# Kernel optimization log

Measured on AMD Instinct MI355X. Metric: run time of the kernel, lower is better.

## Reference

```python
import jax, jax.numpy as jnp
import numpy as np

N = 100000      # nodes
E = 3200000     # edges (avg degree 32)
DU = 256        # unary_channels
DP = 256        # pairwise_channels (== out_channels, required by fusion cat)
H = 64          # hidden_channels = out_channels // 4
DO = 256        # out_channels
STEPS = 1
EPS = 1e-5      # BatchNorm eps (torch default)


def _bn(h, gamma, beta):
    # BatchNorm1d, training-mode batch stats (biased variance, as torch normalizes)
    mu = jnp.mean(h, axis=0)
    var = jnp.var(h, axis=0)
    return gamma * (h - mu) * jax.lax.rsqrt(var + EPS) + beta


def setup_inputs() -> dict:
    key = jax.random.key(0)
    ks = jax.random.split(key, 12)
    edge_index = jax.random.randint(ks[0], (2, E), 0, N, dtype=jnp.int64)
    return {
        "x": jax.random.normal(ks[1], (N, DU), dtype=jnp.float32),
        "y": jax.random.normal(ks[2], (N, DP), dtype=jnp.float32),
        "pos": jax.random.normal(ks[3], (N, 3), dtype=jnp.float32),
        "edge_index": edge_index,
        "Wu": jax.random.normal(ks[4], (DU, H), dtype=jnp.float32) / np.sqrt(DU),
        "gu": jnp.ones((H,), jnp.float32), "bu": jnp.zeros((H,), jnp.float32),
        "Wp": jax.random.normal(ks[5], (DP, H), dtype=jnp.float32) / np.sqrt(DP),
        "gp": jnp.ones((H,), jnp.float32), "bp": jnp.zeros((H,), jnp.float32),
        "c": jnp.eye(H, dtype=jnp.float32) + 0.1 * jax.random.normal(ks[6], (H, H), dtype=jnp.float32),
        "Wm": jax.random.normal(ks[7], (H, DO), dtype=jnp.float32) / np.sqrt(H),
        "gm": jnp.ones((DO,), jnp.float32), "bm": jnp.zeros((DO,), jnp.float32),
        "Wf": jax.random.normal(ks[8], (2 * DO, DO), dtype=jnp.float32) / np.sqrt(2 * DO),
        "gf": jnp.ones((DO,), jnp.float32), "bf": jnp.zeros((DO,), jnp.float32),
    }


def reference(x, y, pos, edge_index, Wu, gu, bu, Wp, gp, bp, c, Wm, gm, bm, Wf, gf, bf):
    i, j = edge_index[0], edge_index[1]
    # unary / pairwise embeddings (Linear no-bias + BN)
    xu = _bn(x @ Wu, gu, bu)                      # [N, H]
    su = _bn(y @ Wp, gp, bp)                      # [N, H]
    # edge logits: -||s_i - s_j||^2, softmax grouped by destination i
    d = su[i] - su[j]                             # [E, H]
    logit = -jnp.sum(d * d, axis=1, keepdims=True)  # [E, 1]
    m = jax.ops.segment_max(logit, i, num_segments=N)
    ex = jnp.exp(logit - m[i])
    denom = jax.ops.segment_sum(ex, i, num_segments=N)
    s = ex / (denom[i] + 1e-16)                   # [E, 1] edge softmax weights
    # CRF mean-field iterations with linear solve
    z = xu
    C = c.T @ c                                   # [H, H]
    Minv = jnp.linalg.inv(jnp.eye(H, dtype=x.dtype) + C)
    h = xu
    for _ in range(STEPS):
        agg = jax.ops.segment_sum(s * h[j], i, num_segments=N)  # gather-scale-scatter
        h = (z + agg @ C) @ Minv
    # output heads
    h = jax.nn.leaky_relu(_bn(h @ Wm, gm, bm))
    out = jax.nn.leaky_relu(_bn(jnp.concatenate([h, y], axis=-1) @ Wf, gf, bf))
    return out
```

## Files before the change

### kernel.cpp

```cpp
#include <hip/hip_runtime.h>
#include <hip/hip_fp16.h>
#include <math.h>

typedef unsigned short u16;
typedef short s16x8 __attribute__((ext_vector_type(8)));
typedef unsigned short u16x8 __attribute__((ext_vector_type(8)));
typedef float f32x4 __attribute__((ext_vector_type(4)));

__device__ __forceinline__ float bf2f(u16 u) {
  unsigned x = ((unsigned)u) << 16;
  return __uint_as_float(x);
}
__device__ __forceinline__ u16 f2bf(float f) {
  unsigned x = __float_as_uint(f);
  unsigned r = x + 0x7FFFu + ((x >> 16) & 1u);
  return (u16)(r >> 16);
}

static const size_t OFF_MINV   = 0;
static const size_t OFF_AU     = 32ull * 1024;
static const size_t OFF_BUE    = 32ull * 1024 + 256;
static const size_t OFF_AP     = 32ull * 1024 + 512;
static const size_t OFF_APBE   = 32ull * 1024 + 768;
static const size_t OFF_AM     = 36ull * 1024;
static const size_t OFF_BM     = 37ull * 1024;
static const size_t OFF_AF     = 38ull * 1024;
static const size_t OFF_BF     = 39ull * 1024;
static const size_t OFF_BTOT   = 40ull * 1024;
static const size_t OFF_BOFF   = 44ull * 1024;
static const size_t OFF_WUT    = 64ull * 1024;
static const size_t OFF_WMT    = 128ull * 1024;
static const size_t OFF_WFT    = 192ull * 1024;
static const size_t OFF_WPH    = 512ull * 1024;
static const size_t OFF_WPL    = 576ull * 1024;
static const size_t OFF_PART1  = 1ull  * 1024 * 1024;
static const size_t OFF_PART2  = 2ull  * 1024 * 1024;
static const size_t OFF_ROWPTR = 3ull  * 1024 * 1024;
static const size_t OFF_BLKCNT = 5ull  * 1024 * 1024;
static const size_t OFF_SRCJ   = 18ull * 1024 * 1024;
static const size_t OFF_U      = 44ull * 1024 * 1024;
static const size_t OFF_P      = 70ull * 1024 * 1024;
static const size_t OFF_PS     = 109ull * 1024 * 1024;
static const size_t OFF_H2     = 122ull * 1024 * 1024;

#define NBLK_BIN 1024

__global__ __launch_bounds__(256) void k_prep(const float* __restrict__ c,
                                              float* __restrict__ minv_out) {
  __shared__ float CC[4096];
  __shared__ float aug[64 * 129];
  __shared__ float fs[64];
  float* cl = aug;
  int t = threadIdx.x;
  for (int idx = t; idx < 4096; idx += 256) cl[idx] = c[idx];
  __syncthreads();
  for (int idx = t; idx < 4096; idx += 256) {
    int a = idx >> 6, b = idx & 63;
    float s = (a == b) ? 1.f : 0.f;
    for (int k = 0; k < 64; ++k) s += cl[k * 64 + a] * cl[k * 64 + b];
    CC[idx] = s;
  }
  __syncthreads();
  for (int idx = t; idx < 8192; idx += 256) {
    int r = idx >> 7, cc = idx & 127;
    aug[r * 129 + cc] = (cc < 64) ? CC[r * 64 + cc] : (((cc - 64) == r) ? 1.f : 0.f);
  }
  __syncthreads();
  int cloc = t & 127;
  int rbase = t >> 7;
  for (int p = 0; p < 64; ++p) {
    float inv = 1.0f / aug[p * 129 + p];
    if (t < 64) fs[t] = (t == p) ? 0.f : aug[t * 129 + p];
    __syncthreads();
    if (t < 128) aug[p * 129 + t] *= inv;
    __syncthreads();
    float pc = aug[p * 129 + cloc];
#pragma unroll
    for (int rr = 0; rr < 64; rr += 2) {
      int r = rr + rbase;
      aug[r * 129 + cloc] -= fs[r] * pc;
    }
    __syncthreads();
  }
  for (int idx = t; idx < 4096; idx += 256) {
    int r = idx >> 6, cc = idx & 63;
    minv_out[idx] = aug[r * 129 + 64 + cc];
  }
}

__global__ __launch_bounds__(256) void k_tcvt_all(const float* __restrict__ Wu, const float* __restrict__ Wm,
                                                  const float* __restrict__ Wf, const float* __restrict__ Wp,
                                                  u16* __restrict__ WUT, u16* __restrict__ WMT,
                                                  u16* __restrict__ WFT, u16* __restrict__ WPH,
                                                  u16* __restrict__ WPL) {
  int b = blockIdx.x, t = threadIdx.x;
  if (b < 64) {
    int i = b * 256 + t;
    int k = i >> 6, n = i & 63;
    WUT[(size_t)n * 256 + k] = f2bf(Wu[i]);
  } else if (b < 128) {
    int i = (b - 64) * 256 + t;
    int k = i >> 8, n = i & 255;
    WMT[(size_t)n * 64 + k] = f2bf(Wm[i]);
  } else if (b < 640) {
    int i = (b - 128) * 256 + t;
    int k = i >> 8, n = i & 255;
    WFT[(size_t)n * 512 + k] = f2bf(Wf[i]);
  } else {
    int i = (b - 640) * 256 + t;
    int k = i >> 6, n = i & 63;
    float v = Wp[i];
    u16 h = f2bf(v);
    WPH[(size_t)n * 256 + k] = h;
    WPL[(size_t)n * 256 + k] = f2bf(v - bf2f(h));
  }
}

__global__ __launch_bounds__(256) void kA1(const int* __restrict__ ei, int E, int chunk,
                                           int* __restrict__ blockCnt, int nbk) {
  __shared__ int c[512];
  int t = threadIdx.x, bid = blockIdx.x;
  c[t] = 0; c[t + 256] = 0;
  __syncthreads();
  int e0 = bid * chunk, e1 = min(E, e0 + chunk);
  for (int e = e0 + t; e < e1; e += 256) atomicAdd(&c[ei[e] >> 8], 1);
  __syncthreads();
  for (int b = t; b < nbk; b += 256) blockCnt[(size_t)bid * nbk + b] = c[b];
}

__global__ __launch_bounds__(256) void kA2(int* __restrict__ blockCnt, int nbk,
                                           int* __restrict__ bucketTot) {
  int b = blockIdx.x, t = threadIdx.x;
  int base = t * 4;
  int v0 = blockCnt[(size_t)(base + 0) * nbk + b];
  int v1 = blockCnt[(size_t)(base + 1) * nbk + b];
  int v2 = blockCnt[(size_t)(base + 2) * nbk + b];
  int v3 = blockCnt[(size_t)(base + 3) * nbk + b];
  int s1 = v0 + v1, s2 = s1 + v2, tot = s2 + v3;
  __shared__ int ps[256];
  ps[t] = tot;
  __syncthreads();
  for (int off = 1; off < 256; off <<= 1) {
    int a = (t >= off) ? ps[t - off] : 0;
    __syncthreads();
    ps[t] += a;
    __syncthreads();
  }
  int ex = (t > 0) ? ps[t - 1] : 0;
  blockCnt[(size_t)(base + 0) * nbk + b] = ex;
  blockCnt[(size_t)(base + 1) * nbk + b] = ex + v0;
  blockCnt[(size_t)(base + 2) * nbk + b] = ex + s1;
  blockCnt[(size_t)(base + 3) * nbk + b] = ex + s2;
  if (t == 255) bucketTot[b] = ps[255];
}

__global__ __launch_bounds__(512) void kA2b(const int* __restrict__ bucketTot,
                                            int* __restrict__ bucketOff, int nbk) {
  __shared__ int s[512];
  int t = threadIdx.x;
  s[t] = (t < nbk) ? bucketTot[t] : 0;
  __syncthreads();
  for (int off = 1; off < 512; off <<= 1) {
    int a = (t >= off) ? s[t - off] : 0;
    __syncthreads();
    s[t] += a;
    __syncthreads();
  }
  if (t == 0) bucketOff[0] = 0;
  if (t < nbk) bucketOff[t + 1] = s[t];
}

__global__ __launch_bounds__(256) void kA3(const int* __restrict__ ei, const int* __restrict__ ej,
                                           int E, int chunk,
                                           const int* __restrict__ blockExc,
                                           const int* __restrict__ bucketOff,
                                           int nbk, unsigned* __restrict__ tmp) {
  __shared__ int c[512], off[512], gb[512], cur[512];
  __shared__ uint2 stage[4096];
  int t = threadIdx.x, bid = blockIdx.x;
  c[t] = 0; c[t + 256] = 0;
  __syncthreads();
  int e0 = bid * chunk, e1 = min(E, e0 + chunk);
  int m = e1 - e0;
  for (int e = e0 + t; e < e1; e += 256) atomicAdd(&c[ei[e] >> 8], 1);
  __syncthreads();
  int v0 = c[t], v1 = c[t + 256];
  off[t] = v0; off[t + 256] = v1;
  __syncthreads();
  for (int o = 1; o < 512; o <<= 1) {
    int a0 = (t >= o) ? off[t - o] : 0;
    int a1 = ((t + 256) >= o) ? off[t + 256 - o] : 0;
    __syncthreads();
    off[t] += a0; off[t + 256] += a1;
    __syncthreads();
  }
  int ex0 = off[t] - v0, ex1 = off[t + 256] - v1;
  if (t < nbk)
    gb[t] = bucketOff[t] + blockExc[(size_t)bid * nbk + t] - ex0;
  if (t + 256 < nbk)
    gb[t + 256] = bucketOff[t + 256] + blockExc[(size_t)bid * nbk + t + 256] - ex1;
  cur[t] = ex0; cur[t + 256] = ex1;
  __syncthreads();
  for (int e = e0 + t; e < e1; e += 256) {
    int i = ei[e];
    int p = atomicAdd(&cur[i >> 8], 1);
    stage[p] = make_uint2((unsigned)i, (unsigned)ej[e]);
  }
  __syncthreads();
  for (int s = t; s < m; s += 256) {
    uint2 v = stage[s];
    tmp[gb[v.x >> 8] + s] = ((v.x & 255u) << 24) | v.y;
  }
}

#define BCAP 12288
__global__ __launch_bounds__(256) void kB(const unsigned* __restrict__ tmp,
                                          const int* __restrict__ bucketOff,
                                          int nbk, int N, int E,
                                          int* __restrict__ rowptr, int* __restrict__ srcj) {
  __shared__ int cnt[256], sc[256], cur[256];
  __shared__ int jbuf[BCAP];
  int b = blockIdx.x, t = threadIdx.x;
  int nb0 = b << 8;
  int e0 = bucketOff[b], e1 = bucketOff[b + 1];
  int m = e1 - e0;
  cnt[t] = 0;
  __syncthreads();
  for (int s = t; s < m; s += 256) atomicAdd(&cnt[tmp[e0 + s] >> 24], 1);
  __syncthreads();
  int v = cnt[t];
  sc[t] = v;
  __syncthreads();
  for (int off = 1; off < 256; off <<= 1) {
    int a = (t >= off) ? sc[t - off] : 0;
    __syncthreads();
    sc[t] += a;
    __syncthreads();
  }
  int exc = sc[t] - v;
  cur[t] = exc;
  if (nb0 + t < N) rowptr[nb0 + t] = e0 + exc;
  if (b == nbk - 1 && t == 0) rowptr[N] = E;
  __syncthreads();
  for (int s = t; s < m; s += 256) {
    unsigned e = tmp[e0 + s];
    int p = atomicAdd(&cur[e >> 24], 1);
    if (p < BCAP) jbuf[p] = (int)(e & 0xFFFFFFu);
  }
  __syncthreads();
  for (int s = t; s < m; s += 256) srcj[e0 + s] = jbuf[s];
}

template<int BN, int AMODE, int OBF, int STATS>
__global__ __launch_bounds__(256) void k_mfma(const u16* __restrict__ Abf, const float* __restrict__ Af32,
                                              int ldA, int K, int M,
                                              const u16* __restrict__ h2, const float* __restrict__ yy,
                                              const float* __restrict__ am, const float* __restrict__ bm,
                                              const u16* __restrict__ Bt,
                                              float* __restrict__ Cf, u16* __restrict__ Cb, int ldC,
                                              int ncTot, float* __restrict__ p1, float* __restrict__ p2) {
  constexpr int WN  = BN / 2;
  constexpr int FN  = WN / 16;
  constexpr int NPB = BN / 32;
  __shared__ u16 lds[2][(128 + BN) * 64];

  int t = threadIdx.x;
  int wid = t >> 6, lane = t & 63;
  int wr = wid >> 1, wc = wid & 1;
  int lr = lane & 15, lk = lane >> 4;
  int m0 = blockIdx.x * 128;
  int n0 = blockIdx.y * BN;
  int nK = K >> 6;

  int sidx = t;
  u16x8 ra[4];
  u16x8 rb[NPB];

  f32x4 acc[4][FN];
#pragma unroll
  for (int m = 0; m < 4; ++m)
#pragma unroll
    for (int n = 0; n < FN; ++n) acc[m][n] = (f32x4){0.f, 0.f, 0.f, 0.f};

  auto loadTile = [&](int kk) {
    int kk0 = kk * 64;
#pragma unroll
    for (int p = 0; p < 4; ++p) {
      int idx = p * 256 + sidx;
      int r = idx >> 3, c8 = idx & 7;
      int row = m0 + r; if (row >= M) row = M - 1;
      int k = kk0 + c8 * 8;
      if constexpr (AMODE == 0) {
        ra[p] = *(const u16x8*)(Abf + (size_t)row * ldA + k);
      } else if constexpr (AMODE == 2) {
        const float* src = Af32 + (size_t)row * ldA + k;
        float4 a = *(const float4*)src;
        float4 b = *(const float4*)(src + 4);
        u16x8 o;
        o[0] = f2bf(a.x); o[1] = f2bf(a.y); o[2] = f2bf(a.z); o[3] = f2bf(a.w);
        o[4] = f2bf(b.x); o[5] = f2bf(b.y); o[6] = f2bf(b.z); o[7] = f2bf(b.w);
        ra[p] = o;
      } else {
        if (kk0 < 256) {
          u16x8 h8 = *(const u16x8*)(h2 + (size_t)row * 256 + k);
          float av[8], bv[8];
          *(float4*)(av)     = *(const float4*)(am + k);
          *(float4*)(av + 4) = *(const float4*)(am + k + 4);
          *(float4*)(bv)     = *(const float4*)(bm + k);
          *(float4*)(bv + 4) = *(const float4*)(bm + k + 4);
          u16x8 o;
#pragma unroll
          for (int j = 0; j < 8; ++j) {
            float v = bf2f((u16)h8[j]) * av[j] + bv[j];
            v = v > 0.f ? v : 0.01f * v;
            o[j] = f2bf(v);
          }
          ra[p] = o;
        } else {
          float yv[8];
          *(float4*)(yv)     = *(const float4*)(yy + (size_t)row * 256 + (k - 256));
          *(float4*)(yv + 4) = *(const float4*)(yy + (size_t)row * 256 + (k - 256) + 4);
          u16x8 o;
#pragma unroll
          for (int j = 0; j < 8; ++j) o[j] = f2bf(yv[j]);
          ra[p] = o;
        }
      }
    }
#pragma unroll
    for (int p = 0; p < NPB; ++p) {
      int idx = p * 256 + sidx;
      int r = idx >> 3, c8 = idx & 7;
      rb[p] = *(const u16x8*)(Bt + (size_t)(n0 + r) * K + kk0 + c8 * 8);
    }
  };

  auto dswrite = [&](int b) {
    char* As  = (char*)&lds[b][0];
    char* Bsc = As + 128 * 64 * 2;
#pragma unroll
    for (int p = 0; p < 4; ++p) {
      int idx = p * 256 + sidx;
      int r = idx >> 3, c8 = idx & 7;
      *(u16x8*)(As + r * 128 + ((c8 * 16) ^ ((r & 7) << 4))) = ra[p];
    }
#pragma unroll
    for (int p = 0; p < NPB; ++p) {
      int idx = p * 256 + sidx;
      int r = idx >> 3, c8 = idx & 7;
      *(u16x8*)(Bsc + r * 128 + ((c8 * 16) ^ ((r & 7) << 4))) = rb[p];
    }
  };

  auto compute = [&](int b) {
    const char* As  = (const char*)&lds[b][0];
    const char* Bsc = As + 128 * 64 * 2;
#pragma unroll
    for (int ks = 0; ks < 2; ++ks) {
      int kb = ks * 64 + lk * 16;
      s16x8 af[4], bfr[FN];
#pragma unroll
      for (int m = 0; m < 4; ++m) {
        int row = wr * 64 + m * 16 + lr;
        af[m] = *(const s16x8*)(As + row * 128 + (kb ^ ((row & 7) << 4)));
      }
#pragma unroll
      for (int n = 0; n < FN; ++n) {
        int row = wc * WN + n * 16 + lr;
        bfr[n] = *(const s16x8*)(Bsc + row * 128 + (kb ^ ((row & 7) << 4)));
      }
#pragma unroll
      for (int m = 0; m < 4; ++m)
#pragma unroll
        for (int n = 0; n < FN; ++n)
          acc[m][n] = __builtin_amdgcn_mfma_f32_16x16x32_bf16(af[m], bfr[n], acc[m][n], 0, 0, 0);
    }
  };

  loadTile(0);
  dswrite(0);
  __syncthreads();
  for (int kk = 0; kk < nK; ++kk) {
    int b = kk & 1;
    if (kk + 1 < nK) loadTile(kk + 1);
    compute(b);
    if (kk + 1 < nK) { dswrite(b ^ 1); __syncthreads(); }
  }

#pragma unroll
  for (int m = 0; m < 4; ++m) {
#pragma unroll
    for (int n = 0; n < FN; ++n) {
      int col = n0 + wc * WN + n * 16 + lr;
#pragma unroll
      for (int q = 0; q < 4; ++q) {
        int row = m0 + wr * 64 + m * 16 + lk * 4 + q;
        if (row < M) {
          if constexpr (OBF) Cb[(size_t)row * ldC + col] = f2bf(acc[m][n][q]);
          else               Cf[(size_t)row * ldC + col] = acc[m][n][q];
        }
      }
    }
  }

  if constexpr (STATS) {
    __syncthreads();
    float* sb = (float*)&lds[0][0];
#pragma unroll
    for (int n = 0; n < FN; ++n) {
      float s1 = 0.f, s2 = 0.f;
#pragma unroll
      for (int m = 0; m < 4; ++m)
#pragma unroll
        for (int q = 0; q < 4; ++q) {
          int row = m0 + wr * 64 + m * 16 + lk * 4 + q;
          float v = (row < M) ? acc[m][n][q] : 0.f;
          s1 += v; s2 += v * v;
        }
      s1 += __shfl_xor(s1, 16); s2 += __shfl_xor(s2, 16);
      s1 += __shfl_xor(s1, 32); s2 += __shfl_xor(s2, 32);
      if (lk == 0) {
        int c = wc * WN + n * 16 + lr;
        sb[(wr * BN + c) * 2 + 0] = s1;
        sb[(wr * BN + c) * 2 + 1] = s2;
      }
    }
    __syncthreads();
    if (t < BN) {
      float s1 = sb[t * 2]     + sb[(BN + t) * 2];
      float s2 = sb[t * 2 + 1] + sb[(BN + t) * 2 + 1];
      p1[(size_t)blockIdx.x * ncTot + n0 + t] = s1;
      p2[(size_t)blockIdx.x * ncTot + n0 + t] = s2;
    }
  }
}

__global__ __launch_bounds__(256) void k_mfma_split(const float* __restrict__ Af, int K, int M,
                                                    const u16* __restrict__ Bh, const u16* __restrict__ Bl,
                                                    float* __restrict__ Cf,
                                                    float* __restrict__ p1, float* __restrict__ p2) {
  __shared__ u16 sAh[128 * 64], sAl[128 * 64], sBh[64 * 64], sBl[64 * 64];
  int t = threadIdx.x;
  int wid = t >> 6, lane = t & 63;
  int wr = wid >> 1, wc = wid & 1;
  int lr = lane & 15, lk = lane >> 4;
  int m0 = blockIdx.x * 128;
  int nK = K >> 6;

  u16x8 rah[4], ral[4], rbh[2], rbl[2];
  f32x4 acc[4][2];
#pragma unroll
  for (int m = 0; m < 4; ++m)
#pragma unroll
    for (int n = 0; n < 2; ++n) acc[m][n] = (f32x4){0.f, 0.f, 0.f, 0.f};

  auto loadTile = [&](int kk) {
    int kk0 = kk * 64;
#pragma unroll
    for (int p = 0; p < 4; ++p) {
      int idx = p * 256 + t;
      int r = idx >> 3, c8 = idx & 7;
      int row = m0 + r; if (row >= M) row = M - 1;
      const float* src = Af + (size_t)row * K + kk0 + c8 * 8;
      float4 a = *(const float4*)src;
      float4 b = *(const float4*)(src + 4);
      float v[8];
      *(float4*)(v) = a; *(float4*)(v + 4) = b;
      u16x8 oh, ol;
#pragma unroll
      for (int j = 0; j < 8; ++j) {
        u16 h = f2bf(v[j]);
        oh[j] = h;
        ol[j] = f2bf(v[j] - bf2f(h));
      }
      rah[p] = oh; ral[p] = ol;
    }
#pragma unroll
    for (int p = 0; p < 2; ++p) {
      int idx = p * 256 + t;
      int r = idx >> 3, c8 = idx & 7;
      rbh[p] = *(const u16x8*)(Bh + (size_t)r * K + kk0 + c8 * 8);
      rbl[p] = *(const u16x8*)(Bl + (size_t)r * K + kk0 + c8 * 8);
    }
  };

  auto dswrite = [&]() {
    char* Ah = (char*)sAh; char* Al = (char*)sAl;
    char* Bhc = (char*)sBh; char* Blc = (char*)sBl;
#pragma unroll
    for (int p = 0; p < 4; ++p) {
      int idx = p * 256 + t;
      int r = idx >> 3, c8 = idx & 7;
      int off = r * 128 + ((c8 * 16) ^ ((r & 7) << 4));
      *(u16x8*)(Ah + off) = rah[p];
      *(u16x8*)(Al + off) = ral[p];
    }
#pragma unroll
    for (int p = 0; p < 2; ++p) {
      int idx = p * 256 + t;
      int r = idx >> 3, c8 = idx & 7;
      int off = r * 128 + ((c8 * 16) ^ ((r & 7) << 4));
      *(u16x8*)(Bhc + off) = rbh[p];
      *(u16x8*)(Blc + off) = rbl[p];
    }
  };

  auto compute = [&]() {
    const char* Ah = (const char*)sAh; const char* Al = (const char*)sAl;
    const char* Bhc = (const char*)sBh; const char* Blc = (const char*)sBl;
#pragma unroll
    for (int ks = 0; ks < 2; ++ks) {
      int kb = ks * 64 + lk * 16;
      s16x8 fah[4], fal[4], fbh[2], fbl[2];
#pragma unroll
      for (int m = 0; m < 4; ++m) {
        int row = wr * 64 + m * 16 + lr;
        int off = row * 128 + (kb ^ ((row & 7) << 4));
        fah[m] = *(const s16x8*)(Ah + off);
        fal[m] = *(const s16x8*)(Al + off);
      }
#pragma unroll
      for (int n = 0; n < 2; ++n) {
        int row = wc * 32 + n * 16 + lr;
        int off = row * 128 + (kb ^ ((row & 7) << 4));
        fbh[n] = *(const s16x8*)(Bhc + off);
        fbl[n] = *(const s16x8*)(Blc + off);
      }
#pragma unroll
      for (int m = 0; m < 4; ++m)
#pragma unroll
        for (int n = 0; n < 2; ++n) {
          acc[m][n] = __builtin_amdgcn_mfma_f32_16x16x32_bf16(fah[m], fbh[n], acc[m][n], 0, 0, 0);
          acc[m][n] = __builtin_amdgcn_mfma_f32_16x16x32_bf16(fah[m], fbl[n], acc[m][n], 0, 0, 0);
          acc[m][n] = __builtin_amdgcn_mfma_f32_16x16x32_bf16(fal[m], fbh[n], acc[m][n], 0, 0, 0);
        }
    }
  };

  loadTile(0);
  for (int kk = 0; kk < nK; ++kk) {
    __syncthreads();
    dswrite();
    __syncthreads();
    if (kk + 1 < nK) loadTile(kk + 1);
    compute();
  }

#pragma unroll
  for (int m = 0; m < 4; ++m) {
#pragma unroll
    for (int n = 0; n < 2; ++n) {
      int col = wc * 32 + n * 16 + lr;
#pragma unroll
      for (int q = 0; q < 4; ++q) {
        int row = m0 + wr * 64 + m * 16 + lk * 4 + q;
        if (row < M) Cf[(size_t)row * 64 + col] = acc[m][n][q];
      }
    }
  }

  __syncthreads();
  float* sb = (float*)sAh;
#pragma unroll
  for (int n = 0; n < 2; ++n) {
    float s1 = 0.f, s2 = 0.f;
#pragma unroll
    for (int m = 0; m < 4; ++m)
#pragma unroll
      for (int q = 0; q < 4; ++q) {
        int row = m0 + wr * 64 + m * 16 + lk * 4 + q;
        float v = (row < M) ? acc[m][n][q] : 0.f;
        s1 += v; s2 += v * v;
      }
    s1 += __shfl_xor(s1, 16); s2 += __shfl_xor(s2, 16);
    s1 += __shfl_xor(s1, 32); s2 += __shfl_xor(s2, 32);
    if (lk == 0) {
      int c = wc * 32 + n * 16 + lr;
      sb[(wr * 64 + c) * 2 + 0] = s1;
      sb[(wr * 64 + c) * 2 + 1] = s2;
    }
  }
  __syncthreads();
  if (t < 64) {
    float s1 = sb[t * 2]     + sb[(64 + t) * 2];
    float s2 = sb[t * 2 + 1] + sb[(64 + t) * 2 + 1];
    p1[(size_t)blockIdx.x * 64 + t] = s1;
    p2[(size_t)blockIdx.x * 64 + t] = s2;
  }
}

__global__ __launch_bounds__(256) void k_reduce_fin(const float* __restrict__ part1,
                                                    const float* __restrict__ part2,
                                                    int nb, int C, float invN,
                                                    const float* __restrict__ gamma,
                                                    const float* __restrict__ beta,
                                                    float* __restrict__ a_out,
                                                    float* __restrict__ b_out) {
  int c = blockIdx.x;
  int t = threadIdx.x;
  float s1 = 0.f, s2 = 0.f;
  for (int b = t; b < nb; b += 256) {
    s1 += part1[(size_t)b * C + c];
    s2 += part2[(size_t)b * C + c];
  }
  for (int m = 32; m; m >>= 1) { s1 += __shfl_xor(s1, m); s2 += __shfl_xor(s2, m); }
  __shared__ float l1[4], l2[4];
  if ((t & 63) == 0) { l1[t >> 6] = s1; l2[t >> 6] = s2; }
  __syncthreads();
  if (t == 0) {
    s1 = l1[0] + l1[1] + l1[2] + l1[3];
    s2 = l2[0] + l2[1] + l2[2] + l2[3];
    float mu  = s1 * invN;
    float var = s2 * invN - mu * mu;
    float a = gamma[c] * rsqrtf(var + 1e-5f);
    a_out[c] = a;
    b_out[c] = beta[c] - mu * a;
  }
}

__global__ __launch_bounds__(256) void k_scaleP(const float* __restrict__ P, const float* __restrict__ ap,
                                                __half* __restrict__ PS, int n8) {
  for (int i = blockIdx.x * 256 + threadIdx.x; i < n8; i += gridDim.x * 256) {
    int c0 = (i & 7) * 8;
    float4 s0 = *(const float4*)(ap + c0), s1 = *(const float4*)(ap + c0 + 4);
    float4 a = ((const float4*)P)[i * 2];
    float4 b = ((const float4*)P)[i * 2 + 1];
    __half2 o0 = __floats2half2_rn(a.x * s0.x, a.y * s0.y);
    __half2 o1 = __floats2half2_rn(a.z * s0.z, a.w * s0.w);
    __half2 o2 = __floats2half2_rn(b.x * s1.x, b.y * s1.y);
    __half2 o3 = __floats2half2_rn(b.z * s1.z, b.w * s1.w);
    uint4 out;
    out.x = *(unsigned*)&o0; out.y = *(unsigned*)&o1;
    out.z = *(unsigned*)&o2; out.w = *(unsigned*)&o3;
    ((uint4*)PS)[i] = out;
  }
}

__global__ __launch_bounds__(256) void k_nodeall(const __half* __restrict__ PS,
                                                 const int* __restrict__ srcj,
                                                 const int* __restrict__ rowptr,
                                                 const u16* __restrict__ UB,
                                                 const float* __restrict__ au,
                                                 const float* __restrict__ bue,
                                                 const float* __restrict__ minv,
                                                 int N, u16* __restrict__ HB) {
  __shared__ float mS[4096];
  __shared__ float zma[4][64];
  int t = threadIdx.x;
  for (int idx = t; idx < 1024; idx += 256)
    ((float4*)mS)[idx] = ((const float4*)minv)[idx];
  __syncthreads();

  int lane = t & 63, wid = t >> 6;
  int node = blockIdx.x * 4 + wid;
  if (node >= N) return;

  int lane8 = lane & 7, g8 = lane >> 3;
  const uint4* P4 = (const uint4*)PS;
  uint4 uv = P4[(size_t)node * 8 + lane8];
  float2 u0 = __half22float2(*(const __half2*)&uv.x);
  float2 u1 = __half22float2(((const __half2*)&uv.x)[1]);
  float2 u2 = __half22float2(*(const __half2*)&uv.z);
  float2 u3 = __half22float2(((const __half2*)&uv.z)[1]);
  float psl = __half2float(PS[(size_t)node * 64 + lane]);
  int b0 = rowptr[node], b1 = rowptr[node + 1];
  int deg = b1 - b0;
  float aggv = 0.f;
  if (deg > 0) {
    int cnt = deg < 64 ? deg : 64;
    int jj = (lane < cnt) ? srcj[b0 + lane] : 0;
    float lg = -INFINITY;
    int capbase = lane & ~7;
    int capsrc  = (lane & 7) << 3;
    for (int ss = 0; ss < cnt; ss += 8) {
      int sl = ss + g8; if (sl >= cnt) sl = cnt - 1;
      int j = __shfl(jj, sl);
      uint4 vv = P4[(size_t)j * 8 + lane8];
      float2 v0 = __half22float2(*(const __half2*)&vv.x);
      float2 v1 = __half22float2(((const __half2*)&vv.x)[1]);
      float2 v2 = __half22float2(*(const __half2*)&vv.z);
      float2 v3 = __half22float2(((const __half2*)&vv.z)[1]);
      float d0 = u0.x - v0.x, d1 = u0.y - v0.y;
      float d2 = u1.x - v1.x, d3 = u1.y - v1.y;
      float d4 = u2.x - v2.x, d5 = u2.y - v2.y;
      float d6 = u3.x - v3.x, d7 = u3.y - v3.y;
      float p = d0*d0 + d1*d1 + d2*d2 + d3*d3 + d4*d4 + d5*d5 + d6*d6 + d7*d7;
      p += __shfl_xor(p, 1, 8);
      p += __shfl_xor(p, 2, 8);
      p += __shfl_xor(p, 4, 8);
      float val = __shfl(p, capsrc);
      if (ss == capbase && lane < cnt) lg = -val;
    }
    float mx = lg;
    for (int s = b0 + 64; s < b1; ++s) {
      int j = srcj[s];
      float d = psl - __half2float(PS[(size_t)j * 64 + lane]);
      float p = d * d;
      for (int m = 32; m; m >>= 1) p += __shfl_xor(p, m);
      mx = fmaxf(mx, -p);
    }
    for (int m = 32; m; m >>= 1) mx = fmaxf(mx, __shfl_xor(mx, m));
    float ex = (lane < cnt) ? __expf(lg - mx) : 0.f;
    float sm = ex;
    for (int s = b0 + 64; s < b1; ++s) {
      int j = srcj[s];
      float d = psl - __half2float(PS[(size_t)j * 64 + lane]);
      float p = d * d;
      for (int m = 32; m; m >>= 1) p += __shfl_xor(p, m);
      if (lane == 0) sm += __expf(-p - mx);
    }
    for (int m = 32; m; m >>= 1) sm += __shfl_xor(sm, m);
    float inv = 1.0f / (sm + 1e-16f);
    float w = ex * inv;
    float acc = 0.f;
    int ss = 0;
    for (; ss + 8 <= cnt; ss += 8) {
      int   j0 = __shfl(jj, ss),     j1 = __shfl(jj, ss + 1);
      int   j2 = __shfl(jj, ss + 2), j3 = __shfl(jj, ss + 3);
      int   j4 = __shfl(jj, ss + 4), j5 = __shfl(jj, ss + 5);
      int   j6 = __shfl(jj, ss + 6), j7 = __shfl(jj, ss + 7);
      float w0 = __shfl(w, ss),      w1 = __shfl(w, ss + 1);
      float w2 = __shfl(w, ss + 2),  w3 = __shfl(w, ss + 3);
      float w4 = __shfl(w, ss + 4),  w5 = __shfl(w, ss + 5);
      float w6 = __shfl(w, ss + 6),  w7 = __shfl(w, ss + 7);
      float v0 = bf2f(UB[(size_t)j0 * 64 + lane]);
      float v1 = bf2f(UB[(size_t)j1 * 64 + lane]);
      float v2 = bf2f(UB[(size_t)j2 * 64 + lane]);
      float v3 = bf2f(UB[(size_t)j3 * 64 + lane]);
      float v4 = bf2f(UB[(size_t)j4 * 64 + lane]);
      float v5 = bf2f(UB[(size_t)j5 * 64 + lane]);
      float v6 = bf2f(UB[(size_t)j6 * 64 + lane]);
      float v7 = bf2f(UB[(size_t)j7 * 64 + lane]);
      acc += w0 * v0 + w1 * v1 + w2 * v2 + w3 * v3;
      acc += w4 * v4 + w5 * v5 + w6 * v6 + w7 * v7;
    }
    for (; ss < cnt; ++ss) {
      int j0 = __shfl(jj, ss);
      float w0 = __shfl(w, ss);
      acc += w0 * bf2f(UB[(size_t)j0 * 64 + lane]);
    }
    for (int s = b0 + 64; s < b1; ++s) {
      int j = srcj[s];
      float d = psl - __half2float(PS[(size_t)j * 64 + lane]);
      float p = d * d;
      for (int m = 32; m; m >>= 1) p += __shfl_xor(p, m);
      acc += __expf(-p - mx) * inv * bf2f(UB[(size_t)j * 64 + lane]);
    }
    aggv = au[lane] * acc + bue[lane];
  }
  float z = au[lane] * bf2f(UB[(size_t)node * 64 + lane]) + bue[lane];
  zma[wid][lane] = z - aggv;
  float h = aggv;
#pragma unroll 8
  for (int k = 0; k < 64; ++k) h += zma[wid][k] * mS[k * 64 + lane];
  HB[(size_t)node * 64 + lane] = f2bf(h);
}

__global__ __launch_bounds__(256) void k_bnact16(const u16* __restrict__ raw, const float* __restrict__ af,
                                                 const float* __restrict__ bfp, float* __restrict__ out, int n8) {
  int i = blockIdx.x * 256 + threadIdx.x;
  int stride = gridDim.x * 256;
  for (; i < n8; i += stride) {
    int c0 = (i & 31) * 8;
    float av[8], bv[8];
    *(float4*)(av) = *(const float4*)(af + c0);  *(float4*)(av + 4) = *(const float4*)(af + c0 + 4);
    *(float4*)(bv) = *(const float4*)(bfp + c0); *(float4*)(bv + 4) = *(const float4*)(bfp + c0 + 4);
    u16x8 r = ((const u16x8*)raw)[i];
    float o[8];
#pragma unroll
    for (int j = 0; j < 8; ++j) {
      float v = bf2f((u16)r[j]) * av[j] + bv[j];
      o[j] = (v > 0.f) ? v : 0.01f * v;
    }
    ((float4*)out)[i * 2]     = *(float4*)(o);
    ((float4*)out)[i * 2 + 1] = *(float4*)(o + 4);
  }
}

extern "C" void kernel_launch(void* const* d_in, const int* in_sizes, int n_in,
                              void* d_out, int out_size, void* d_ws, size_t ws_size,
                              hipStream_t stream) {
  const float* x    = (const float*)d_in[0];
  const float* y    = (const float*)d_in[1];
  const int*   eidx = (const int*)d_in[3];
  const float* Wu   = (const float*)d_in[4];
  const float* gu   = (const float*)d_in[5];
  const float* bu   = (const float*)d_in[6];
  const float* Wp   = (const float*)d_in[7];
  const float* gp   = (const float*)d_in[8];
  const float* bp   = (const float*)d_in[9];
  const float* cIn  = (const float*)d_in[10];
  const float* Wm   = (const float*)d_in[11];
  const float* gm   = (const float*)d_in[12];
  const float* bm   = (const float*)d_in[13];
  const float* Wf   = (const float*)d_in[14];
  const float* gf   = (const float*)d_in[15];
  const float* bfv  = (const float*)d_in[16];

  const int N = in_sizes[0] / 256;
  const int E = in_sizes[3] / 2;
  const int* ei = eidx;
  const int* ej = eidx + E;

  char* ws = (char*)d_ws;
  float* MINV  = (float*)(ws + OFF_MINV);
  float* AU    = (float*)(ws + OFF_AU);
  float* BUE   = (float*)(ws + OFF_BUE);
  float* AP    = (float*)(ws + OFF_AP);
  float* APBE  = (float*)(ws + OFF_APBE);
  float* AM    = (float*)(ws + OFF_AM);
  float* BM    = (float*)(ws + OFF_BM);
  float* AF    = (float*)(ws + OFF_AF);
  float* BF    = (float*)(ws + OFF_BF);
  int*   BTOT  = (int*)(ws + OFF_BTOT);
  int*   BOFF  = (int*)(ws + OFF_BOFF);
  u16*   WUT   = (u16*)(ws + OFF_WUT);
  u16*   WMT   = (u16*)(ws + OFF_WMT);
  u16*   WFT   = (u16*)(ws + OFF_WFT);
  u16*   WPH   = (u16*)(ws + OFF_WPH);
  u16*   WPL   = (u16*)(ws + OFF_WPL);
  float* PART1 = (float*)(ws + OFF_PART1);
  float* PART2 = (float*)(ws + OFF_PART2);
  int*   ROWPTR= (int*)(ws + OFF_ROWPTR);
  int*   BLKCNT= (int*)(ws + OFF_BLKCNT);
  u16*   HB    = (u16*)(ws + OFF_BLKCNT);
  int*   SRCJ  = (int*)(ws + OFF_SRCJ);
  u16*   RAWO  = (u16*)(ws + OFF_SRCJ);
  u16*   UBRAW = (u16*)(ws + OFF_U);
  unsigned* TMP= (unsigned*)(ws + OFF_P);
  float* P     = (float*)(ws + OFF_P);
  __half* PS   = (__half*)(ws + OFF_PS);
  u16*   H2    = (u16*)(ws + OFF_H2);

  const float invN = 1.0f / (float)N;
  const int mtiles   = (N + 127) / 128;
  const int n8_64    = N * 64 / 8;
  const int n8_256   = N * 256 / 8;
  const int nbk      = (N + 255) >> 8;
  const int chunk    = (E + NBLK_BIN - 1) / NBLK_BIN;

  k_prep<<<1, 256, 0, stream>>>(cIn, MINV);
  k_tcvt_all<<<704, 256, 0, stream>>>(Wu, Wm, Wf, Wp, WUT, WMT, WFT, WPH, WPL);

  kA1<<<NBLK_BIN, 256, 0, stream>>>(ei, E, chunk, BLKCNT, nbk);
  kA2<<<nbk, 256, 0, stream>>>(BLKCNT, nbk, BTOT);
  kA2b<<<1, 512, 0, stream>>>(BTOT, BOFF, nbk);
  kA3<<<NBLK_BIN, 256, 0, stream>>>(ei, ej, E, chunk, BLKCNT, BOFF, nbk, TMP);
  kB<<<nbk, 256, 0, stream>>>(TMP, BOFF, nbk, N, E, ROWPTR, SRCJ);

  k_mfma<64, 2, 1, 1><<<dim3(mtiles, 1), 256, 0, stream>>>(
      nullptr, x, 256, 256, N, nullptr, nullptr, nullptr, nullptr, WUT,
      nullptr, UBRAW, 64, 64, PART1, PART2);
  k_reduce_fin<<<64, 256, 0, stream>>>(PART1, PART2, mtiles, 64, invN, gu, bu, AU, BUE);

  k_mfma_split<<<mtiles, 256, 0, stream>>>(y, 256, N, WPH, WPL, P, PART1, PART2);
  k_reduce_fin<<<64, 256, 0, stream>>>(PART1, PART2, mtiles, 64, invN, gp, bp, AP, APBE);
  k_scaleP<<<1024, 256, 0, stream>>>(P, AP, PS, n8_64);

  k_nodeall<<<(N + 3) / 4, 256, 0, stream>>>(PS, SRCJ, ROWPTR, UBRAW, AU, BUE, MINV, N, HB);

  k_mfma<128, 0, 1, 1><<<dim3(mtiles, 2), 256, 0, stream>>>(
      HB, nullptr, 64, 64, N, nullptr, nullptr, nullptr, nullptr, WMT,
      nullptr, H2, 256, 256, PART1, PART2);
  k_reduce_fin<<<256, 256, 0, stream>>>(PART1, PART2, mtiles, 256, invN, gm, bm, AM, BM);

  k_mfma<128, 1, 1, 1><<<dim3(mtiles, 2), 256, 0, stream>>>(
      nullptr, nullptr, 0, 512, N, H2, y, AM, BM, WFT,
      nullptr, RAWO, 256, 256, PART1, PART2);
  k_reduce_fin<<<256, 256, 0, stream>>>(PART1, PART2, mtiles, 256, invN, gf, bfv, AF, BF);
  k_bnact16<<<2048, 256, 0, stream>>>(RAWO, AF, BF, (float*)d_out, n8_256);
}
```

Measured before the change: 550.5 us.

## Use fp16 MFMA for pairwise GEMM, widen output GEMM tiles, merge BN reductions

The pairwise embedding GEMM drops the three-pass bf16 hi/lo split and runs as a single fp16 MFMA pass. The two output-head GEMMs move to a new 512-thread kernel whose block covers all 256 output columns, so the A tile is loaded once per row block instead of twice. The two 64-channel BN reductions are merged into one launch, and the matrix inverse folds the pivot normalisation into a final per-row divide. The aim is to cut MFMA work, redundant A-tile loads and launch count, at the cost of fp16 rounding in the edge-logit embedding, which could hurt softmax accuracy.

```diff
diff --git a/kernel.cpp b/kernel.cpp
--- a/kernel.cpp
+++ b/kernel.cpp
@@ -5,6 +5,7 @@
 typedef unsigned short u16;
 typedef short s16x8 __attribute__((ext_vector_type(8)));
 typedef unsigned short u16x8 __attribute__((ext_vector_type(8)));
+typedef _Float16 f16x8 __attribute__((ext_vector_type(8)));
 typedef float f32x4 __attribute__((ext_vector_type(4)));
 
 __device__ __forceinline__ float bf2f(u16 u) {
@@ -15,6 +16,10 @@
   unsigned x = __float_as_uint(f);
   unsigned r = x + 0x7FFFu + ((x >> 16) & 1u);
   return (u16)(r >> 16);
+}
+__device__ __forceinline__ u16 f2h(float f) {
+  __half h = __float2half_rn(f);
+  return *reinterpret_cast<u16*>(&h);
 }
 
 static const size_t OFF_MINV   = 0;
@@ -32,9 +37,10 @@
 static const size_t OFF_WMT    = 128ull * 1024;
 static const size_t OFF_WFT    = 192ull * 1024;
 static const size_t OFF_WPH    = 512ull * 1024;
-static const size_t OFF_WPL    = 576ull * 1024;
-static const size_t OFF_PART1  = 1ull  * 1024 * 1024;
-static const size_t OFF_PART2  = 2ull  * 1024 * 1024;
+static const size_t OFF_PART1A = 1ull  * 1024 * 1024;
+static const size_t OFF_PART1B = 1ull  * 1024 * 1024 + 512 * 1024;
+static const size_t OFF_PART2A = 2ull  * 1024 * 1024;
+static const size_t OFF_PART2B = 2ull  * 1024 * 1024 + 512 * 1024;
 static const size_t OFF_ROWPTR = 3ull  * 1024 * 1024;
 static const size_t OFF_BLKCNT = 5ull  * 1024 * 1024;
 static const size_t OFF_SRCJ   = 18ull * 1024 * 1024;
@@ -69,10 +75,7 @@
   int cloc = t & 127;
   int rbase = t >> 7;
   for (int p = 0; p < 64; ++p) {
-    float inv = 1.0f / aug[p * 129 + p];
-    if (t < 64) fs[t] = (t == p) ? 0.f : aug[t * 129 + p];
-    __syncthreads();
-    if (t < 128) aug[p * 129 + t] *= inv;
+    if (t < 64) fs[t] = (t == p) ? 0.f : aug[t * 129 + p] / aug[p * 129 + p];
     __syncthreads();
     float pc = aug[p * 129 + cloc];
 #pragma unroll
@@ -84,15 +87,14 @@
   }
   for (int idx = t; idx < 4096; idx += 256) {
     int r = idx >> 6, cc = idx & 63;
-    minv_out[idx] = aug[r * 129 + 64 + cc];
+    minv_out[idx] = aug[r * 129 + 64 + cc] / aug[r * 129 + r];
   }
 }
 
 __global__ __launch_bounds__(256) void k_tcvt_all(const float* __restrict__ Wu, const float* __restrict__ Wm,
                                                   const float* __restrict__ Wf, const float* __restrict__ Wp,
                                                   u16* __restrict__ WUT, u16* __restrict__ WMT,
-                                                  u16* __restrict__ WFT, u16* __restrict__ WPH,
-                                                  u16* __restrict__ WPL) {
+                                                  u16* __restrict__ WFT, u16* __restrict__ WPH) {
   int b = blockIdx.x, t = threadIdx.x;
   if (b < 64) {
     int i = b * 256 + t;
@@ -109,10 +111,7 @@
   } else {
     int i = (b - 640) * 256 + t;
     int k = i >> 6, n = i & 63;
-    float v = Wp[i];
-    u16 h = f2bf(v);
-    WPH[(size_t)n * 256 + k] = h;
-    WPL[(size_t)n * 256 + k] = f2bf(v - bf2f(h));
+    WPH[(size_t)n * 256 + k] = f2h(Wp[i]);
   }
 }
 
@@ -251,11 +250,9 @@
   for (int s = t; s < m; s += 256) srcj[e0 + s] = jbuf[s];
 }
 
-template<int BN, int AMODE, int OBF, int STATS>
+template<int BN, int AMODE, int OBF, int STATS, int FP16>
 __global__ __launch_bounds__(256) void k_mfma(const u16* __restrict__ Abf, const float* __restrict__ Af32,
                                               int ldA, int K, int M,
-                                              const u16* __restrict__ h2, const float* __restrict__ yy,
-                                              const float* __restrict__ am, const float* __restrict__ bm,
                                               const u16* __restrict__ Bt,
                                               float* __restrict__ Cf, u16* __restrict__ Cb, int ldC,
                                               int ncTot, float* __restrict__ p1, float* __restrict__ p2) {
@@ -292,39 +289,19 @@
       int k = kk0 + c8 * 8;
       if constexpr (AMODE == 0) {
         ra[p] = *(const u16x8*)(Abf + (size_t)row * ldA + k);
-      } else if constexpr (AMODE == 2) {
+      } else {
         const float* src = Af32 + (size_t)row * ldA + k;
         float4 a = *(const float4*)src;
         float4 b = *(const float4*)(src + 4);
         u16x8 o;
-        o[0] = f2bf(a.x); o[1] = f2bf(a.y); o[2] = f2bf(a.z); o[3] = f2bf(a.w);
-        o[4] = f2bf(b.x); o[5] = f2bf(b.y); o[6] = f2bf(b.z); o[7] = f2bf(b.w);
+        if constexpr (FP16) {
+          o[0] = f2h(a.x); o[1] = f2h(a.y); o[2] = f2h(a.z); o[3] = f2h(a.w);
+          o[4] = f2h(b.x); o[5] = f2h(b.y); o[6] = f2h(b.z); o[7] = f2h(b.w);
+        } else {
+          o[0] = f2bf(a.x); o[1] = f2bf(a.y); o[2] = f2bf(a.z); o[3] = f2bf(a.w);
+          o[4] = f2bf(b.x); o[5] = f2bf(b.y); o[6] = f2bf(b.z); o[7] = f2bf(b.w);
+        }
         ra[p] = o;
-      } else {
-        if (kk0 < 256) {
-          u16x8 h8 = *(const u16x8*)(h2 + (size_t)row * 256 + k);
-          float av[8], bv[8];
-          *(float4*)(av)     = *(const float4*)(am + k);
-          *(float4*)(av + 4) = *(const float4*)(am + k + 4);
-          *(float4*)(bv)     = *(const float4*)(bm + k);
-          *(float4*)(bv + 4) = *(const float4*)(bm + k + 4);
-          u16x8 o;
-#pragma unroll
-          for (int j = 0; j < 8; ++j) {
-            float v = bf2f((u16)h8[j]) * av[j] + bv[j];
-            v = v > 0.f ? v : 0.01f * v;
-            o[j] = f2bf(v);
-          }
-          ra[p] = o;
-        } else {
-          float yv[8];
-          *(float4*)(yv)     = *(const float4*)(yy + (size_t)row * 256 + (k - 256));
-          *(float4*)(yv + 4) = *(const float4*)(yy + (size_t)row * 256 + (k - 256) + 4);
-          u16x8 o;
-#pragma unroll
-          for (int j = 0; j < 8; ++j) o[j] = f2bf(yv[j]);
-          ra[p] = o;
-        }
       }
     }
 #pragma unroll
@@ -358,22 +335,25 @@
 #pragma unroll
     for (int ks = 0; ks < 2; ++ks) {
       int kb = ks * 64 + lk * 16;
-      s16x8 af[4], bfr[FN];
 #pragma unroll
       for (int m = 0; m < 4; ++m) {
-        int row = wr * 64 + m * 16 + lr;
-        af[m] = *(const s16x8*)(As + row * 128 + (kb ^ ((row & 7) << 4)));
+        int rowA = wr * 64 + m * 16 + lr;
+        const char* pa = As + rowA * 128 + (kb ^ ((rowA & 7) << 4));
+#pragma unroll
+        for (int n = 0; n < FN; ++n) {
+          int rowB = wc * WN + n * 16 + lr;
+          const char* pb = Bsc + rowB * 128 + (kb ^ ((rowB & 7) << 4));
+          if constexpr (FP16) {
+            f16x8 af = *(const f16x8*)pa;
+            f16x8 bf = *(const f16x8*)pb;
+            acc[m][n] = __builtin_amdgcn_mfma_f32_16x16x32_f16(af, bf, acc[m][n], 0, 0, 0);
+          } else {
+            s16x8 af = *(const s16x8*)pa;
+            s16x8 bf = *(const s16x8*)pb;
+            acc[m][n] = __builtin_amdgcn_mfma_f32_16x16x32_bf16(af, bf, acc[m][n], 0, 0, 0);
+          }
+        }
       }
-#pragma unroll
-      for (int n = 0; n < FN; ++n) {
-        int row = wc * WN + n * 16 + lr;
-        bfr[n] = *(const s16x8*)(Bsc + row * 128 + (kb ^ ((row & 7) << 4)));
-      }
-#pragma unroll
-      for (int m = 0; m < 4; ++m)
-#pragma unroll
-        for (int n = 0; n < FN; ++n)
-          acc[m][n] = __builtin_amdgcn_mfma_f32_16x16x32_bf16(af[m], bfr[n], acc[m][n], 0, 0, 0);
     }
   };
 
@@ -435,105 +415,113 @@
   }
 }
 
-__global__ __launch_bounds__(256) void k_mfma_split(const float* __restrict__ Af, int K, int M,
-                                                    const u16* __restrict__ Bh, const u16* __restrict__ Bl,
-                                                    float* __restrict__ Cf,
-                                                    float* __restrict__ p1, float* __restrict__ p2) {
-  __shared__ u16 sAh[128 * 64], sAl[128 * 64], sBh[64 * 64], sBl[64 * 64];
+template<int AMODE>
+__global__ __launch_bounds__(512) void k_mfma2(const u16* __restrict__ Abf, int ldA, int K, int M,
+                                               const u16* __restrict__ h2, const float* __restrict__ yy,
+                                               const float* __restrict__ am, const float* __restrict__ bm,
+                                               const u16* __restrict__ Bt,
+                                               u16* __restrict__ Cb,
+                                               float* __restrict__ p1, float* __restrict__ p2) {
+  __shared__ u16 lds[(128 + 256) * 64];
   int t = threadIdx.x;
   int wid = t >> 6, lane = t & 63;
-  int wr = wid >> 1, wc = wid & 1;
+  int wr = wid >> 2, wc = wid & 3;
   int lr = lane & 15, lk = lane >> 4;
   int m0 = blockIdx.x * 128;
   int nK = K >> 6;
 
-  u16x8 rah[4], ral[4], rbh[2], rbl[2];
-  f32x4 acc[4][2];
+  u16x8 ra[2];
+  u16x8 rb[4];
+  f32x4 acc[4][4];
 #pragma unroll
   for (int m = 0; m < 4; ++m)
 #pragma unroll
-    for (int n = 0; n < 2; ++n) acc[m][n] = (f32x4){0.f, 0.f, 0.f, 0.f};
+    for (int n = 0; n < 4; ++n) acc[m][n] = (f32x4){0.f, 0.f, 0.f, 0.f};
 
   auto loadTile = [&](int kk) {
     int kk0 = kk * 64;
 #pragma unroll
-    for (int p = 0; p < 4; ++p) {
-      int idx = p * 256 + t;
+    for (int p = 0; p < 2; ++p) {
+      int idx = p * 512 + t;
       int r = idx >> 3, c8 = idx & 7;
       int row = m0 + r; if (row >= M) row = M - 1;
-      const float* src = Af + (size_t)row * K + kk0 + c8 * 8;
-      float4 a = *(const float4*)src;
-      float4 b = *(const float4*)(src + 4);
-      float v[8];
-      *(float4*)(v) = a; *(float4*)(v + 4) = b;
-      u16x8 oh, ol;
-#pragma unroll
-      for (int j = 0; j < 8; ++j) {
-        u16 h = f2bf(v[j]);
-        oh[j] = h;
-        ol[j] = f2bf(v[j] - bf2f(h));
+      int k = kk0 + c8 * 8;
+      if constexpr (AMODE == 0) {
+        ra[p] = *(const u16x8*)(Abf + (size_t)row * ldA + k);
+      } else {
+        if (kk0 < 256) {
+          u16x8 h8 = *(const u16x8*)(h2 + (size_t)row * 256 + k);
+          float av[8], bv[8];
+          *(float4*)(av)     = *(const float4*)(am + k);
+          *(float4*)(av + 4) = *(const float4*)(am + k + 4);
+          *(float4*)(bv)     = *(const float4*)(bm + k);
+          *(float4*)(bv + 4) = *(const float4*)(bm + k + 4);
+          u16x8 o;
+#pragma unroll
+          for (int j = 0; j < 8; ++j) {
+            float v = bf2f((u16)h8[j]) * av[j] + bv[j];
+            v = v > 0.f ? v : 0.01f * v;
+            o[j] = f2bf(v);
+          }
+          ra[p] = o;
+        } else {
+          float yv[8];
+          *(float4*)(yv)     = *(const float4*)(yy + (size_t)row * 256 + (k - 256));
+          *(float4*)(yv + 4) = *(const float4*)(yy + (size_t)row * 256 + (k - 256) + 4);
+          u16x8 o;
+#pragma unroll
+          for (int j = 0; j < 8; ++j) o[j] = f2bf(yv[j]);
+          ra[p] = o;
+        }
       }
-      rah[p] = oh; ral[p] = ol;
-    }
+    }
+#pragma unroll
+    for (int p = 0; p < 4; ++p) {
+      int idx = p * 512 + t;
+      int r = idx >> 3, c8 = idx & 7;
+      rb[p] = *(const u16x8*)(Bt + (size_t)r * K + kk0 + c8 * 8);
+    }
+  };
+
+  auto dswrite = [&]() {
+    char* As  = (char*)&lds[0];
+    char* Bsc = As + 128 * 64 * 2;
 #pragma unroll
     for (int p = 0; p < 2; ++p) {
-      int idx = p * 256 + t;
+      int idx = p * 512 + t;
       int r = idx >> 3, c8 = idx & 7;
-      rbh[p] = *(const u16x8*)(Bh + (size_t)r * K + kk0 + c8 * 8);
-      rbl[p] = *(const u16x8*)(Bl + (size_t)r * K + kk0 + c8 * 8);
+      *(u16x8*)(As + r * 128 + ((c8 * 16) ^ ((r & 7) << 4))) = ra[p];
+    }
+#pragma unroll
+    for (int p = 0; p < 4; ++p) {
+      int idx = p * 512 + t;
+      int r = idx >> 3, c8 = idx & 7;
+      *(u16x8*)(Bsc + r * 128 + ((c8 * 16) ^ ((r & 7) << 4))) = rb[p];
     }
   };
 
-  auto dswrite = [&]() {
-    char* Ah = (char*)sAh; char* Al = (char*)sAl;
-    char* Bhc = (char*)sBh; char* Blc = (char*)sBl;
-#pragma unroll
-    for (int p = 0; p < 4; ++p) {
-      int idx = p * 256 + t;
-      int r = idx >> 3, c8 = idx & 7;
-      int off = r * 128 + ((c8 * 16) ^ ((r & 7) << 4));
-      *(u16x8*)(Ah + off) = rah[p];
-      *(u16x8*)(Al + off) = ral[p];
-    }
-#pragma unroll
-    for (int p = 0; p < 2; ++p) {
-      int idx = p * 256 + t;
-      int r = idx >> 3, c8 = idx & 7;
-      int off = r * 128 + ((c8 * 16) ^ ((r & 7) << 4));
-      *(u16x8*)(Bhc + off) = rbh[p];
-      *(u16x8*)(Blc + off) = rbl[p];
-    }
-  };
-
   auto compute = [&]() {
-    const char* Ah = (const char*)sAh; const char* Al = (const char*)sAl;
-    const char* Bhc = (const char*)sBh; const char* Blc = (const char*)sBl;
+    const char* As  = (const char*)&lds[0];
+    const char* Bsc = As + 128 * 64 * 2;
 #pragma unroll
     for (int ks = 0; ks < 2; ++ks) {
       int kb = ks * 64 + lk * 16;
-      s16x8 fah[4], fal[4], fbh[2], fbl[2];
+      s16x8 af[4], bfr[4];
 #pragma unroll
       for (int m = 0; m < 4; ++m) {
         int row = wr * 64 + m * 16 + lr;
-        int off = row * 128 + (kb ^ ((row & 7) << 4));
-        fah[m] = *(const s16x8*)(Ah + off);
-        fal[m] = *(const s16x8*)(Al + off);
+        af[m] = *(const s16x8*)(As + row * 128 + (kb ^ ((row & 7) << 4)));
       }
 #pragma unroll
-      for (int n = 0; n < 2; ++n) {
-        int row = wc * 32 + n * 16 + lr;
-        int off = row * 128 + (kb ^ ((row & 7) << 4));
-        fbh[n] = *(const s16x8*)(Bhc + off);
-        fbl[n] = *(const s16x8*)(Blc + off);
+      for (int n = 0; n < 4; ++n) {
+        int row = wc * 64 + n * 16 + lr;
+        bfr[n] = *(const s16x8*)(Bsc + row * 128 + (kb ^ ((row & 7) << 4)));
       }
 #pragma unroll
       for (int m = 0; m < 4; ++m)
 #pragma unroll
-        for (int n = 0; n < 2; ++n) {
-          acc[m][n] = __builtin_amdgcn_mfma_f32_16x16x32_bf16(fah[m], fbh[n], acc[m][n], 0, 0, 0);
-          acc[m][n] = __builtin_amdgcn_mfma_f32_16x16x32_bf16(fah[m], fbl[n], acc[m][n], 0, 0, 0);
-          acc[m][n] = __builtin_amdgcn_mfma_f32_16x16x32_bf16(fal[m], fbh[n], acc[m][n], 0, 0, 0);
-        }
+        for (int n = 0; n < 4; ++n)
+          acc[m][n] = __builtin_amdgcn_mfma_f32_16x16x32_bf16(af[m], bfr[n], acc[m][n], 0, 0, 0);
     }
   };
 
@@ -549,20 +537,20 @@
 #pragma unroll
   for (int m = 0; m < 4; ++m) {
 #pragma unroll
-    for (int n = 0; n < 2; ++n) {
-      int col = wc * 32 + n * 16 + lr;
+    for (int n = 0; n < 4; ++n) {
+      int col = wc * 64 + n * 16 + lr;
 #pragma unroll
       for (int q = 0; q < 4; ++q) {
         int row = m0 + wr * 64 + m * 16 + lk * 4 + q;
-        if (row < M) Cf[(size_t)row * 64 + col] = acc[m][n][q];
+        if (row < M) Cb[(size_t)row * 256 + col] = f2bf(acc[m][n][q]);
       }
     }
   }
 
   __syncthreads();
-  float* sb = (float*)sAh;
-#pragma unroll
-  for (int n = 0; n < 2; ++n) {
+  float* sb = (float*)&lds[0];
+#pragma unroll
+  for (int n = 0; n < 4; ++n) {
     float s1 = 0.f, s2 = 0.f;
 #pragma unroll
     for (int m = 0; m < 4; ++m)
@@ -575,17 +563,55 @@
     s1 += __shfl_xor(s1, 16); s2 += __shfl_xor(s2, 16);
     s1 += __shfl_xor(s1, 32); s2 += __shfl_xor(s2, 32);
     if (lk == 0) {
-      int c = wc * 32 + n * 16 + lr;
-      sb[(wr * 64 + c) * 2 + 0] = s1;
-      sb[(wr * 64 + c) * 2 + 1] = s2;
-    }
-  }
-  __syncthreads();
-  if (t < 64) {
-    float s1 = sb[t * 2]     + sb[(64 + t) * 2];
-    float s2 = sb[t * 2 + 1] + sb[(64 + t) * 2 + 1];
-    p1[(size_t)blockIdx.x * 64 + t] = s1;
-    p2[(size_t)blockIdx.x * 64 + t] = s2;
+      int c = wc * 64 + n * 16 + lr;
+      sb[(wr * 256 + c) * 2 + 0] = s1;
+      sb[(wr * 256 + c) * 2 + 1] = s2;
+    }
+  }
+  __syncthreads();
+  if (t < 256) {
+    float s1 = sb[t * 2]     + sb[(256 + t) * 2];
+    float s2 = sb[t * 2 + 1] + sb[(256 + t) * 2 + 1];
+    p1[(size_t)blockIdx.x * 256 + t] = s1;
+    p2[(size_t)blockIdx.x * 256 + t] = s2;
+  }
+}
+
+__global__ __launch_bounds__(256) void k_reduce2(const float* __restrict__ p1a, const float* __restrict__ p2a,
+                                                 const float* __restrict__ p1b, const float* __restrict__ p2b,
+                                                 int nb, float invN,
+                                                 const float* __restrict__ gu, const float* __restrict__ bu,
+                                                 const float* __restrict__ gp, const float* __restrict__ bp,
+                                                 float* __restrict__ AU, float* __restrict__ BUE,
+                                                 float* __restrict__ AP, float* __restrict__ APBE) {
+  int isB = blockIdx.x >> 6;
+  int c = blockIdx.x & 63;
+  int t = threadIdx.x;
+  const float* part1 = isB ? p1b : p1a;
+  const float* part2 = isB ? p2b : p2a;
+  float s1 = 0.f, s2 = 0.f;
+  for (int b = t; b < nb; b += 256) {
+    s1 += part1[(size_t)b * 64 + c];
+    s2 += part2[(size_t)b * 64 + c];
+  }
+  for (int m = 32; m; m >>= 1) { s1 += __shfl_xor(s1, m); s2 += __shfl_xor(s2, m); }
+  __shared__ float l1[4], l2[4];
+  if ((t & 63) == 0) { l1[t >> 6] = s1; l2[t >> 6] = s2; }
+  __syncthreads();
+  if (t == 0) {
+    s1 = l1[0] + l1[1] + l1[2] + l1[3];
+    s2 = l2[0] + l2[1] + l2[2] + l2[3];
+    float mu  = s1 * invN;
+    float var = s2 * invN - mu * mu;
+    if (isB) {
+      float a = gp[c] * rsqrtf(var + 1e-5f);
+      AP[c] = a;
+      APBE[c] = bp[c] - mu * a;
+    } else {
+      float a = gu[c] * rsqrtf(var + 1e-5f);
+      AU[c] = a;
+      BUE[c] = bu[c] - mu * a;
+    }
   }
 }
 
@@ -818,9 +844,10 @@
   u16*   WMT   = (u16*)(ws + OFF_WMT);
   u16*   WFT   = (u16*)(ws + OFF_WFT);
   u16*   WPH   = (u16*)(ws + OFF_WPH);
-  u16*   WPL   = (u16*)(ws + OFF_WPL);
-  float* PART1 = (float*)(ws + OFF_PART1);
-  float* PART2 = (float*)(ws + OFF_PART2);
+  float* PART1A= (float*)(ws + OFF_PART1A);
+  float* PART1B= (float*)(ws + OFF_PART1B);
+  float* PART2A= (float*)(ws + OFF_PART2A);
+  float* PART2B= (float*)(ws + OFF_PART2B);
   int*   ROWPTR= (int*)(ws + OFF_ROWPTR);
   int*   BLKCNT= (int*)(ws + OFF_BLKCNT);
   u16*   HB    = (u16*)(ws + OFF_BLKCNT);
@@ -840,7 +867,7 @@
   const int chunk    = (E + NBLK_BIN - 1) / NBLK_BIN;
 
   k_prep<<<1, 256, 0, stream>>>(cIn, MINV);
-  k_tcvt_all<<<704, 256, 0, stream>>>(Wu, Wm, Wf, Wp, WUT, WMT, WFT, WPH, WPL);
+  k_tcvt_all<<<704, 256, 0, stream>>>(Wu, Wm, Wf, Wp, WUT, WMT, WFT, WPH);
 
   kA1<<<NBLK_BIN, 256, 0, stream>>>(ei, E, chunk, BLKCNT, nbk);
   kA2<<<nbk, 256, 0, stream>>>(BLKCNT, nbk, BTOT);
@@ -848,25 +875,24 @@
   kA3<<<NBLK_BIN, 256, 0, stream>>>(ei, ej, E, chunk, BLKCNT, BOFF, nbk, TMP);
   kB<<<nbk, 256, 0, stream>>>(TMP, BOFF, nbk, N, E, ROWPTR, SRCJ);
 
-  k_mfma<64, 2, 1, 1><<<dim3(mtiles, 1), 256, 0, stream>>>(
-      nullptr, x, 256, 256, N, nullptr, nullptr, nullptr, nullptr, WUT,
-      nullptr, UBRAW, 64, 64, PART1, PART2);
-  k_reduce_fin<<<64, 256, 0, stream>>>(PART1, PART2, mtiles, 64, invN, gu, bu, AU, BUE);
-
-  k_mfma_split<<<mtiles, 256, 0, stream>>>(y, 256, N, WPH, WPL, P, PART1, PART2);
-  k_reduce_fin<<<64, 256, 0, stream>>>(PART1, PART2, mtiles, 64, invN, gp, bp, AP, APBE);
+  k_mfma<64, 2, 1, 1, 0><<<dim3(mtiles, 1), 256, 0, stream>>>(
+      nullptr, x, 256, 256, N, WUT, nullptr, UBRAW, 64, 64, PART1A, PART2A);
+
+  k_mfma<64, 2, 0, 1, 1><<<dim3(mtiles, 1), 256, 0, stream>>>(
+      nullptr, y, 256, 256, N, WPH, P, nullptr, 64, 64, PART1B, PART2B);
+
+  k_reduce2<<<128, 256, 0, stream>>>(PART1A, PART2A, PART1B, PART2B, mtiles, invN,
+                                     gu, bu, gp, bp, AU, BUE, AP, APBE);
   k_scaleP<<<1024, 256, 0, stream>>>(P, AP, PS, n8_64);
 
   k_nodeall<<<(N + 3) / 4, 256, 0, stream>>>(PS, SRCJ, ROWPTR, UBRAW, AU, BUE, MINV, N, HB);
 
-  k_mfma<128, 0, 1, 1><<<dim3(mtiles, 2), 256, 0, stream>>>(
-      HB, nullptr, 64, 64, N, nullptr, nullptr, nullptr, nullptr, WMT,
-      nullptr, H2, 256, 256, PART1, PART2);
-  k_reduce_fin<<<256, 256, 0, stream>>>(PART1, PART2, mtiles, 256, invN, gm, bm, AM, BM);
-
-  k_mfma<128, 1, 1, 1><<<dim3(mtiles, 2), 256, 0, stream>>>(
-      nullptr, nullptr, 0, 512, N, H2, y, AM, BM, WFT,
-      nullptr, RAWO, 256, 256, PART1, PART2);
-  k_reduce_fin<<<256, 256, 0, stream>>>(PART1, PART2, mtiles, 256, invN, gf, bfv, AF, BF);
+  k_mfma2<0><<<mtiles, 512, 0, stream>>>(
+      HB, 64, 64, N, nullptr, nullptr, nullptr, nullptr, WMT, H2, PART1A, PART2A);
+  k_reduce_fin<<<256, 256, 0, stream>>>(PART1A, PART2A, mtiles, 256, invN, gm, bm, AM, BM);
+
+  k_mfma2<1><<<mtiles, 512, 0, stream>>>(
+      nullptr, 0, 512, N, H2, y, AM, BM, WFT, RAWO, PART1A, PART2A);
+  k_reduce_fin<<<256, 256, 0, stream>>>(PART1A, PART2A, mtiles, 256, invN, gf, bfv, AF, BF);
   k_bnact16<<<2048, 256, 0, stream>>>(RAWO, AF, BF, (float*)d_out, n8_256);
 }
```

After: 527.3 us. -4.2%, faster.
